# Kernel optimization log

Measured on AMD Instinct MI355X. Metric: run time of the kernel, lower is better.

The kernel has to match this reference:

```python
import jax, jax.numpy as jnp
import numpy as np

B, S, HID = 2, 2048, 2048
NH, HD = 16, 128
KVC, QC = 512, 1536


def _rope(x):
    # x: [B, H, S, D]; interleaved-pair rotation matching the torch view(..., D//2, 2)
    b, h, s, d = x.shape
    inv_freq = 1.0 / (10000.0 ** (jnp.arange(0, d, 2, dtype=jnp.float32) / d))  # [D/2]
    pos = jnp.arange(s, dtype=jnp.float32)
    sinusoid = pos[:, None] * inv_freq[None, :]  # [S, D/2]
    sin = jnp.sin(sinusoid)[None, None]  # [1,1,S,D/2]
    cos = jnp.cos(sinusoid)[None, None]
    xr = x.reshape(b, h, s, d // 2, 2)
    x1, x2 = xr[..., 0], xr[..., 1]
    out = jnp.stack([x1 * cos - x2 * sin, x1 * sin + x2 * cos], axis=-1)
    return out.reshape(b, h, s, d)


def setup_inputs() -> dict:
    key = jax.random.key(0)
    ks = jax.random.split(key, 14)
    def lin(k, fan_in, fan_out):
        lim = 1.0 / np.sqrt(fan_in)
        kw, kb = jax.random.split(k)
        W = jax.random.uniform(kw, (fan_in, fan_out), jnp.float32, -lim, lim)
        b = jax.random.uniform(kb, (fan_out,), jnp.float32, -lim, lim)
        return W, b
    x = jax.random.normal(ks[0], (B, S, HID), jnp.float32)
    # causal mask (positions with 0 are masked out)
    attention_mask = jnp.tril(jnp.ones((S, S), jnp.int32))[None, None]  # [1,1,S,S]
    W_dkv, b_dkv = lin(ks[1], HID, KVC)
    W_uk, b_uk = lin(ks[2], KVC, NH * HD)
    W_uv, b_uv = lin(ks[3], KVC, NH * HD)
    W_dq, b_dq = lin(ks[4], HID, QC)
    W_uq, b_uq = lin(ks[5], QC, NH * HD)
    W_o, b_o = lin(ks[6], NH * HD, HID)
    return dict(x=x, attention_mask=attention_mask,
                W_dkv=W_dkv, b_dkv=b_dkv, W_uk=W_uk, b_uk=b_uk,
                W_uv=W_uv, b_uv=b_uv, W_dq=W_dq, b_dq=b_dq,
                W_uq=W_uq, b_uq=b_uq, W_o=W_o, b_o=b_o)


def reference(x, attention_mask, W_dkv, b_dkv, W_uk, b_uk, W_uv, b_uv,
              W_dq, b_dq, W_uq, b_uq, W_o, b_o):
    b, s, _ = x.shape
    kv = x @ W_dkv + b_dkv                                   # [B,S,KVC]
    k = (kv @ W_uk + b_uk).reshape(b, s, NH, HD).transpose(0, 2, 1, 3)  # [B,H,S,D]
    v = (kv @ W_uv + b_uv).reshape(b, s, NH, HD).transpose(0, 2, 1, 3)
    q = ((x @ W_dq + b_dq) @ W_uq + b_uq).reshape(b, s, NH, HD).transpose(0, 2, 1, 3)
    q, k = _rope(q), _rope(k)
    scores = jnp.einsum('bhqd,bhkd->bhqk', q, k) / jnp.sqrt(jnp.float32(HD))
    scores = jnp.where(attention_mask == 0, jnp.float32(-1e9), scores)
    probs = jax.nn.softmax(scores, axis=-1)
    out = jnp.einsum('bhqk,bhkd->bhqd', probs, v)            # [B,H,S,D]
    out = out.transpose(0, 2, 1, 3).reshape(b, s, NH * HD)
    return out @ W_o + b_o
```

## Files before the change

kernel.cpp:

```cpp
#include <hip/hip_runtime.h>
#include <stdint.h>

typedef unsigned short u16;
typedef uint32_t u32;
typedef __attribute__((ext_vector_type(8))) short short8;
typedef __attribute__((ext_vector_type(4))) float f32x4;
typedef __attribute__((ext_vector_type(4))) u32 u32x4;
typedef __attribute__((ext_vector_type(2))) u32 u32x2;
typedef __attribute__((ext_vector_type(4))) unsigned short u16x4;

#define BS_ 4096
#define S_ 2048
#define HID_ 2048

__device__ __forceinline__ float bf2f(u16 u) { union { u32 i; float f; } v; v.i = ((u32)u) << 16; return v.f; }
__device__ __forceinline__ u16 f2bf(float f) {
  union { float f; u32 i; } v; v.f = f;
  u32 r = v.i + 0x7fffu + ((v.i >> 16) & 1u);
  return (u16)(r >> 16);
}

__device__ __forceinline__ void gload16(const void* gsrc, void* ldst) {
  __builtin_amdgcn_global_load_lds(
      (const __attribute__((address_space(1))) void*)gsrc,
      (__attribute__((address_space(3))) void*)ldst, 16, 0, 0);
}

__global__ __launch_bounds__(256) void prep(const float* __restrict__ x, u16* __restrict__ xb,
                                            const float* __restrict__ W_dkv, const float* __restrict__ W_dq,
                                            const float* __restrict__ W_uk, const float* __restrict__ W_uv,
                                            const float* __restrict__ W_uq, const float* __restrict__ W_o,
                                            u16* __restrict__ WdkvqT, u16* __restrict__ WukvT,
                                            u16* __restrict__ WuqT, u16* __restrict__ WoT,
                                            const float* __restrict__ b_dkv, const float* __restrict__ b_dq,
                                            const float* __restrict__ b_uk, const float* __restrict__ b_uv,
                                            float* __restrict__ cs, float* __restrict__ bc1,
                                            float* __restrict__ bc2) {
  __shared__ float tile[64][65];
  int b = blockIdx.x;
  const int t = threadIdx.x;
  if (b < 8192) {
    int i = b * 256 + t;
    float4 v = ((const float4*)x)[i];
    u16x4 o;
    o.x = f2bf(v.x); o.y = f2bf(v.y); o.z = f2bf(v.z); o.w = f2bf(v.w);
    ((u16x4*)xb)[i] = o;
    return;
  }
  b -= 8192;
  if (b < 3328) {
    const float* W; u16* WT; int K, N, gx, r = b;
    if (r < 256)                 { W = W_dkv; WT = WdkvqT;                    K = 2048; N = 512;  gx = 8;  }
    else if ((r -= 256) < 768)   { W = W_dq;  WT = WdkvqT + (size_t)512 * 2048; K = 2048; N = 1536; gx = 24; }
    else if ((r -= 768) < 256)   { W = W_uk;  WT = WukvT;                     K = 512;  N = 2048; gx = 32; }
    else if ((r -= 256) < 256)   { W = W_uv;  WT = WukvT + (size_t)2048 * 512;  K = 512;  N = 2048; gx = 32; }
    else if ((r -= 256) < 768)   { W = W_uq;  WT = WuqT;                      K = 1536; N = 2048; gx = 32; }
    else                         { r -= 768;  W = W_o; WT = WoT;              K = 2048; N = 2048; gx = 32; }
    const int nb = (r % gx) * 64, kb = (r / gx) * 64;
#pragma unroll
    for (int c = 0; c < 4; ++c) {
      int idx = c * 256 + t;
      int row = idx >> 4;
      int col4 = (idx & 15) * 4;
      float4 v = *(const float4*)&W[(size_t)(kb + row) * N + nb + col4];
      tile[row][col4 + 0] = v.x; tile[row][col4 + 1] = v.y;
      tile[row][col4 + 2] = v.z; tile[row][col4 + 3] = v.w;
    }
    __syncthreads();
#pragma unroll
    for (int c = 0; c < 4; ++c) {
      int idx = c * 256 + t;
      int n = idx >> 4;
      int k4 = (idx & 15) * 4;
      u16x4 o;
      o.x = f2bf(tile[k4 + 0][n]); o.y = f2bf(tile[k4 + 1][n]);
      o.z = f2bf(tile[k4 + 2][n]); o.w = f2bf(tile[k4 + 3][n]);
      *(u16x4*)&WT[(size_t)(nb + n) * K + kb + k4] = o;
    }
    return;
  }
  b -= 3328;
  if (b < 512) {
    int idx = b * 256 + t;
    int pos = idx >> 6, i = idx & 63;
    float inv = powf(10000.f, -(float)i / 64.f);
    float a = (float)pos * inv;
    cs[idx * 2] = cosf(a);
    cs[idx * 2 + 1] = sinf(a);
    return;
  }
  b -= 512;
  {
    int i = b * 256 + t;
    if (i < 512) bc1[i] = b_dkv[i];
    else if (i < 2048) bc1[i] = b_dq[i - 512];
    else if (i < 4096) bc2[i - 2048] = b_uk[i - 2048];
    else if (i < 6144) bc2[i - 2048] = b_uv[i - 4096];
  }
}

template <int OUTF32>
__global__ __launch_bounds__(256) void gemm_bt(const u16* __restrict__ A, int lda,
                                               const u16* __restrict__ BT,
                                               const float* __restrict__ bias,
                                               void* __restrict__ Cout,
                                               int M, int N, int K) {
  __shared__ u16 As[128 * 64];
  __shared__ u16 Bs[128 * 64];
  const int t = threadIdx.x;
  const int lane = t & 63, wave = t >> 6;
  const int wm = wave >> 1, wn = wave & 1;
  const int gx = gridDim.x;
  const int nwg = gx * gridDim.y;
  const int flat = blockIdx.y * gx + blockIdx.x;
  const int swz = (flat & 7) * (nwg >> 3) + (flat >> 3);
  const int tn = swz % gx, tm = swz / gx;
  const int r16 = lane & 15, q4 = lane >> 4;

  f32x4 acc[4][4];
#pragma unroll
  for (int m = 0; m < 4; ++m)
#pragma unroll
    for (int n = 0; n < 4; ++n) acc[m][n] = (f32x4){0.f, 0.f, 0.f, 0.f};

  for (int kt = 0; kt < K; kt += 64) {
#pragma unroll
    for (int c = 0; c < 4; ++c) {
      int idx = c * 256 + t;
      int row = idx >> 3, ch = idx & 7;
      gload16(&A[(size_t)(tm * 128 + row) * lda + kt + ch * 8], (char*)As + idx * 16);
      gload16(&BT[(size_t)(tn * 128 + row) * K + kt + ch * 8], (char*)Bs + idx * 16);
    }
    __syncthreads();
#pragma unroll
    for (int kk = 0; kk < 64; kk += 32) {
      short8 af[4], bfv[4];
#pragma unroll
      for (int m = 0; m < 4; ++m)
        af[m] = *(const short8*)&As[(wm * 64 + m * 16 + r16) * 64 + kk + q4 * 8];
#pragma unroll
      for (int n = 0; n < 4; ++n)
        bfv[n] = *(const short8*)&Bs[(wn * 64 + n * 16 + r16) * 64 + kk + q4 * 8];
      __builtin_amdgcn_s_setprio(1);
#pragma unroll
      for (int m = 0; m < 4; ++m)
#pragma unroll
        for (int n = 0; n < 4; ++n)
          acc[m][n] = __builtin_amdgcn_mfma_f32_16x16x32_bf16(bfv[n], af[m], acc[m][n], 0, 0, 0);
      __builtin_amdgcn_s_setprio(0);
    }
    __syncthreads();
  }
#pragma unroll
  for (int n = 0; n < 4; ++n) {
    int gc0 = tn * 128 + wn * 64 + n * 16 + q4 * 4;
    float4 bv4 = *(const float4*)&bias[gc0];
#pragma unroll
    for (int m = 0; m < 4; ++m) {
      int grow = tm * 128 + wm * 64 + m * 16 + r16;
      float v0 = acc[m][n][0] + bv4.x, v1 = acc[m][n][1] + bv4.y;
      float v2 = acc[m][n][2] + bv4.z, v3 = acc[m][n][3] + bv4.w;
      if (OUTF32) {
        float4 o; o.x = v0; o.y = v1; o.z = v2; o.w = v3;
        *(float4*)&((float*)Cout)[(size_t)grow * N + gc0] = o;
      } else {
        u16x4 o; o.x = f2bf(v0); o.y = f2bf(v1); o.z = f2bf(v2); o.w = f2bf(v3);
        *(u16x4*)&((u16*)Cout)[(size_t)grow * N + gc0] = o;
      }
    }
  }
}

__global__ __launch_bounds__(256) void gemm23(const u16* __restrict__ kvq1,
                                              const u16* __restrict__ WukvT, const u16* __restrict__ WuqT,
                                              const float* __restrict__ bc2, const float* __restrict__ b_uq,
                                              const float* __restrict__ cs,
                                              u16* __restrict__ kbuf, u16* __restrict__ VT,
                                              u16* __restrict__ qb) {
  __shared__ u16 As[128 * 64];
  __shared__ u16 Bs[128 * 64];
  const int t = threadIdx.x;
  const int lane = t & 63, wave = t >> 6;
  const int wm = wave >> 1, wn = wave & 1;
  const int bflat = blockIdx.x;
  const bool g2 = (bflat < 1024);
  const u16* A  = g2 ? kvq1 : (kvq1 + 512);
  const u16* BT = g2 ? WukvT : WuqT;
  const float* bias = g2 ? bc2 : b_uq;
  const int N = g2 ? 4096 : 2048;
  const int K = g2 ? 512 : 1536;
  const int gx = g2 ? 32 : 16;
  const int nwg = g2 ? 1024 : 512;
  const int flat = g2 ? bflat : (bflat - 1024);
  const int swz = (flat & 7) * (nwg >> 3) + (flat >> 3);
  const int tn = swz % gx, tm = swz / gx;
  const int r16 = lane & 15, q4 = lane >> 4;

  f32x4 acc[4][4];
#pragma unroll
  for (int m = 0; m < 4; ++m)
#pragma unroll
    for (int n = 0; n < 4; ++n) acc[m][n] = (f32x4){0.f, 0.f, 0.f, 0.f};

  for (int kt = 0; kt < K; kt += 64) {
#pragma unroll
    for (int c = 0; c < 4; ++c) {
      int idx = c * 256 + t;
      int row = idx >> 3, ch = idx & 7;
      gload16(&A[(size_t)(tm * 128 + row) * 2048 + kt + ch * 8], (char*)As + idx * 16);
      gload16(&BT[(size_t)(tn * 128 + row) * K + kt + ch * 8], (char*)Bs + idx * 16);
    }
    __syncthreads();
#pragma unroll
    for (int kk = 0; kk < 64; kk += 32) {
      short8 af[4], bfv[4];
#pragma unroll
      for (int m = 0; m < 4; ++m)
        af[m] = *(const short8*)&As[(wm * 64 + m * 16 + r16) * 64 + kk + q4 * 8];
#pragma unroll
      for (int n = 0; n < 4; ++n)
        bfv[n] = *(const short8*)&Bs[(wn * 64 + n * 16 + r16) * 64 + kk + q4 * 8];
      __builtin_amdgcn_s_setprio(1);
#pragma unroll
      for (int m = 0; m < 4; ++m)
#pragma unroll
        for (int n = 0; n < 4; ++n)
          acc[m][n] = __builtin_amdgcn_mfma_f32_16x16x32_bf16(bfv[n], af[m], acc[m][n], 0, 0, 0);
      __builtin_amdgcn_s_setprio(0);
    }
    __syncthreads();
  }

  const bool isV = g2 && (tn >= 16);
  u16* outp = g2 ? kbuf : qb;
#pragma unroll
  for (int n = 0; n < 4; ++n) {
    int gc0 = tn * 128 + wn * 64 + n * 16 + q4 * 4;
    float4 bv4 = *(const float4*)&bias[gc0];
    const int i0 = (gc0 & 127) >> 1;
#pragma unroll
    for (int m = 0; m < 4; ++m) {
      int grow = tm * 128 + wm * 64 + m * 16 + r16;
      float v0 = acc[m][n][0] + bv4.x, v1 = acc[m][n][1] + bv4.y;
      float v2 = acc[m][n][2] + bv4.z, v3 = acc[m][n][3] + bv4.w;
      if (!isV) {
        int s = grow & 2047;
        float4 cp = *(const float4*)&cs[((size_t)s * 64 + i0) * 2];
        float y0 = v0 * cp.x - v1 * cp.y;
        float y1 = v0 * cp.y + v1 * cp.x;
        float y2 = v2 * cp.z - v3 * cp.w;
        float y3 = v2 * cp.w + v3 * cp.z;
        u16x4 o; o.x = f2bf(y0); o.y = f2bf(y1); o.z = f2bf(y2); o.w = f2bf(y3);
        *(u16x4*)&outp[(size_t)grow * 2048 + gc0] = o;
      } else {
        int gcv = gc0 - 2048;
        int hh = gcv >> 7, d0 = gcv & 127;
        int bb = grow >> 11, s = grow & 2047;
        u16* vdst = VT + ((size_t)(bb * 16 + hh) * 128 + d0) * S_ + s;
        vdst[0]        = f2bf(v0);
        vdst[S_]       = f2bf(v1);
        vdst[2 * S_]   = f2bf(v2);
        vdst[3 * S_]   = f2bf(v3);
      }
    }
  }
}

__global__ __launch_bounds__(256, 2) void attn_kernel(const u16* __restrict__ Q, const u16* __restrict__ K,
                                                      int kld, const u16* __restrict__ VT,
                                                      u16* __restrict__ O) {
  __shared__ char smem[75776];
  u16* Kl = (u16*)smem;
  u16* Vl = (u16*)(smem + 32768);
  u16* Pl = (u16*)(smem + 65536);
  float* ex = (float*)smem;

  const int t = threadIdx.x;
  const int lane = t & 63, w = t >> 6;
  const int r16 = lane & 15, q4 = lane >> 4;
  const int par = w >> 1, sub = w & 1;
  const int b = blockIdx.x;
  const int xcd = b & 7, u = b >> 3;
  const int p = u & 15, g4 = u >> 4;
  const int bh = g4 * 8 + xcd;
  const int bb = bh >> 4, h = bh & 15;
  const u16* Qb = Q + (size_t)bb * S_ * HID_ + (size_t)h * 128;
  const u16* Kb = K + (size_t)bb * S_ * kld + (size_t)h * 128;
  const u16* VTb = VT + (size_t)bh * 128 * S_;
  u16* Ob = O + (size_t)bb * S_ * HID_ + (size_t)h * 128;

  auto stage = [&](int rs, int kvbase) {
#pragma unroll
    for (int pp = 0; pp < 2; ++pp) {
      int kvb = kvbase + pp * 32;
      char* kd = (char*)(Kl + (size_t)(rs * 2 + pp) * 4096);
      char* vd = (char*)(Vl + (size_t)(rs * 2 + pp) * 4096);
#pragma unroll
      for (int c = 0; c < 2; ++c) {
        int s = c * 256 + t;
        int row = s >> 4;
        int ch = (s & 15) ^ (row & 7);
        gload16(&Kb[(size_t)(kvb + row) * kld + ch * 8], kd + s * 16);
      }
#pragma unroll
      for (int c = 0; c < 2; ++c) {
        int s = c * 256 + t;
        int row = s >> 2;
        int ch = (s & 3) ^ ((row >> 1) & 3);
        gload16(&VTb[(size_t)row * S_ + kvb + ch * 8], vd + s * 16);
      }
    }
  };

  u16* Pw = Pl + (size_t)w * 1280;
  const float SCALE = 0.08838834764831845f;

#pragma unroll
  for (int seg = 0; seg < 2; ++seg) {
    const int qt = seg ? (31 - p) : p;
    const int nr = qt + 1;
    const int qrow0 = qt * 64 + sub * 32;

    short8 qf[2][4];
#pragma unroll
    for (int m = 0; m < 2; ++m)
#pragma unroll
      for (int dk = 0; dk < 4; ++dk)
        qf[m][dk] = *(const short8*)&Qb[(size_t)(qrow0 + m * 16 + r16) * HID_ + dk * 32 + q4 * 8];

    f32x4 ao[2][8];
    float mr[2], lr[2];
#pragma unroll
    for (int m = 0; m < 2; ++m) {
#pragma unroll
      for (int dn = 0; dn < 8; ++dn) ao[m][dn] = (f32x4){0.f, 0.f, 0.f, 0.f};
      mr[m] = -1e30f; lr[m] = 0.f;
    }

    stage(0, 0);
    __syncthreads();

    for (int r = 0; r < nr; ++r) {
      const int rs = r & 1;
      if (r + 1 < nr) stage(rs ^ 1, (r + 1) * 64);
      const int kv0 = r * 64 + par * 32;
      const u16* Kbuf = Kl + (size_t)(rs * 2 + par) * 4096;
      const u16* Vbuf = Vl + (size_t)(rs * 2 + par) * 4096;

      if (kv0 <= qrow0 + 31) {
        f32x4 sc[2][2];
#pragma unroll
        for (int m = 0; m < 2; ++m)
#pragma unroll
          for (int n = 0; n < 2; ++n) sc[m][n] = (f32x4){0.f, 0.f, 0.f, 0.f};
#pragma unroll
        for (int dk = 0; dk < 4; ++dk) {
          short8 kf[2];
#pragma unroll
          for (int n = 0; n < 2; ++n) {
            int kr = n * 16 + r16;
            int ba = (kr * 256 + dk * 64 + q4 * 16) ^ ((kr & 7) << 4);
            kf[n] = *(const short8*)((const char*)Kbuf + ba);
          }
          __builtin_amdgcn_s_setprio(1);
#pragma unroll
          for (int n = 0; n < 2; ++n)
#pragma unroll
            for (int m = 0; m < 2; ++m)
              sc[m][n] = __builtin_amdgcn_mfma_f32_16x16x32_bf16(kf[n], qf[m][dk], sc[m][n], 0, 0, 0);
          __builtin_amdgcn_s_setprio(0);
        }
        const bool nm = (kv0 + 31 > qrow0);
#pragma unroll
        for (int m = 0; m < 2; ++m) {
          const int q = qrow0 + m * 16 + r16;
#pragma unroll
          for (int n = 0; n < 2; ++n)
#pragma unroll
            for (int j = 0; j < 4; ++j) {
              float sv = sc[m][n][j] * SCALE;
              if (nm) {
                int kv = kv0 + n * 16 + q4 * 4 + j;
                if (kv > q) sv = -1e30f;
              }
              sc[m][n][j] = sv;
            }
        }
        float tm0[2];
#pragma unroll
        for (int m = 0; m < 2; ++m) {
          float tm = sc[m][0][0];
#pragma unroll
          for (int n = 0; n < 2; ++n)
#pragma unroll
            for (int j = 0; j < 4; ++j) tm = fmaxf(tm, sc[m][n][j]);
          tm = fmaxf(tm, __shfl_xor(tm, 16));
          tm = fmaxf(tm, __shfl_xor(tm, 32));
          tm0[m] = tm;
        }
        float growth = fmaxf(tm0[0] - mr[0], tm0[1] - mr[1]);
        if (!__all(growth <= 8.0f)) {
#pragma unroll
          for (int m = 0; m < 2; ++m) {
            float mnew = fmaxf(mr[m], tm0[m]);
            float fsc = __expf(mr[m] - mnew);
            lr[m] *= fsc; mr[m] = mnew;
#pragma unroll
            for (int dn = 0; dn < 8; ++dn) ao[m][dn] *= fsc;
          }
        }
#pragma unroll
        for (int m = 0; m < 2; ++m) {
          float ps = 0.f;
#pragma unroll
          for (int n = 0; n < 2; ++n)
#pragma unroll
            for (int j = 0; j < 4; ++j) {
              float pv = __expf(sc[m][n][j] - mr[m]);
              sc[m][n][j] = pv;
              ps += pv;
            }
          ps += __shfl_xor(ps, 16);
          ps += __shfl_xor(ps, 32);
          lr[m] += ps;
        }
#pragma unroll
        for (int m = 0; m < 2; ++m)
#pragma unroll
          for (int n = 0; n < 2; ++n) {
            u32 lo, hi;
            asm("v_cvt_pk_bf16_f32 %0, %1, %2" : "=v"(lo) : "v"(sc[m][n][0]), "v"(sc[m][n][1]));
            asm("v_cvt_pk_bf16_f32 %0, %1, %2" : "=v"(hi) : "v"(sc[m][n][2]), "v"(sc[m][n][3]));
            u32x2 pr; pr.x = lo; pr.y = hi;
            int ba = (m * 16 + r16) * 80 + n * 32 + q4 * 8;
            *(u32x2*)((char*)Pw + ba) = pr;
          }
        short8 pb[2];
#pragma unroll
        for (int m = 0; m < 2; ++m)
          pb[m] = *(const short8*)((const char*)Pw + (m * 16 + r16) * 80 + q4 * 16);
        __builtin_amdgcn_s_setprio(1);
#pragma unroll
        for (int dn = 0; dn < 8; ++dn) {
          int d = dn * 16 + r16;
          int bv = d * 64 + ((q4 ^ ((d >> 1) & 3)) * 16);
          short8 vf = *(const short8*)((const char*)Vbuf + bv);
#pragma unroll
          for (int m = 0; m < 2; ++m)
            ao[m][dn] = __builtin_amdgcn_mfma_f32_16x16x32_bf16(vf, pb[m], ao[m][dn], 0, 0, 0);
        }
        __builtin_amdgcn_s_setprio(0);
      }
      __syncthreads();
    }

    {
      float* exb = ex + (size_t)sub * 4352 + (size_t)lane * 68;
      if (par == 1) {
#pragma unroll
        for (int m = 0; m < 2; ++m)
#pragma unroll
          for (int dn = 0; dn < 8; ++dn)
            *(f32x4*)(exb + m * 32 + dn * 4) = ao[m][dn];
        exb[64] = mr[0]; exb[65] = mr[1]; exb[66] = lr[0]; exb[67] = lr[1];
      }
      __syncthreads();
      if (par == 0) {
#pragma unroll
        for (int m = 0; m < 2; ++m) {
          float mB = exb[64 + m], lB = exb[66 + m];
          float mx = fmaxf(mr[m], mB);
          float wA = __expf(mr[m] - mx), wB = __expf(mB - mx);
          float inv = 1.f / (lr[m] * wA + lB * wB);
          const int q = qrow0 + m * 16 + r16;
#pragma unroll
          for (int dn = 0; dn < 8; ++dn) {
            f32x4 ob = *(const f32x4*)(exb + m * 32 + dn * 4);
            u16x4 o;
#pragma unroll
            for (int j = 0; j < 4; ++j) o[j] = f2bf((ao[m][dn][j] * wA + ob[j] * wB) * inv);
            *(u16x4*)&Ob[(size_t)q * HID_ + dn * 16 + q4 * 4] = o;
          }
        }
      }
      __syncthreads();
    }
  }
}

extern "C" void kernel_launch(void* const* d_in, const int* in_sizes, int n_in,
                              void* d_out, int out_size, void* d_ws, size_t ws_size,
                              hipStream_t stream) {
  (void)in_sizes; (void)n_in; (void)out_size; (void)ws_size;
  const float* x     = (const float*)d_in[0];
  const float* W_dkv = (const float*)d_in[2];
  const float* b_dkv = (const float*)d_in[3];
  const float* W_uk  = (const float*)d_in[4];
  const float* b_uk  = (const float*)d_in[5];
  const float* W_uv  = (const float*)d_in[6];
  const float* b_uv  = (const float*)d_in[7];
  const float* W_dq  = (const float*)d_in[8];
  const float* b_dq  = (const float*)d_in[9];
  const float* W_uq  = (const float*)d_in[10];
  const float* b_uq  = (const float*)d_in[11];
  const float* W_o   = (const float*)d_in[12];
  const float* b_o   = (const float*)d_in[13];
  float* out = (float*)d_out;

  char* ws = (char*)d_ws;
  size_t off = 0;
  auto carve = [&](size_t bytes) { void* p = ws + off; off += (bytes + 255) & ~(size_t)255; return p; };
  u16* xb     = (u16*)carve((size_t)BS_ * 2048 * 2);
  u16* WdkvqT = (u16*)carve((size_t)2048 * 2048 * 2);
  u16* WukvT  = (u16*)carve((size_t)4096 * 512 * 2);
  u16* WuqT   = (u16*)carve((size_t)2048 * 1536 * 2);
  u16* WoT    = (u16*)carve((size_t)2048 * 2048 * 2);
  u16* kvq1   = (u16*)carve((size_t)BS_ * 2048 * 2);
  u16* kbuf   = (u16*)carve((size_t)BS_ * 2048 * 2);
  u16* qb     = (u16*)carve((size_t)BS_ * 2048 * 2);
  u16* aob    = (u16*)carve((size_t)BS_ * 2048 * 2);
  float* cs   = (float*)carve((size_t)2048 * 64 * 2 * 4);
  float* bc1  = (float*)carve((size_t)2048 * 4);
  float* bc2  = (float*)carve((size_t)4096 * 4);
  u16* VT     = xb;

  prep<<<dim3(12056), 256, 0, stream>>>(x, xb, W_dkv, W_dq, W_uk, W_uv, W_uq, W_o,
                                        WdkvqT, WukvT, WuqT, WoT,
                                        b_dkv, b_dq, b_uk, b_uv, cs, bc1, bc2);

  gemm_bt<0><<<dim3(2048 / 128, BS_ / 128), 256, 0, stream>>>(xb, 2048, WdkvqT, bc1, kvq1, BS_, 2048, 2048);

  gemm23<<<dim3(1536), 256, 0, stream>>>(kvq1, WukvT, WuqT, bc2, b_uq, cs, kbuf, VT, qb);

  attn_kernel<<<dim3(512), 256, 0, stream>>>(qb, kbuf, 2048, VT, aob);

  gemm_bt<1><<<dim3(2048 / 128, BS_ / 128), 256, 0, stream>>>(aob, 2048, WoT, b_o, out, BS_, 2048, 2048);
}
```

Before: 271.3 us.

## Double-buffer gemm_bt K tiles and transpose V through LDS for coalesced stores

Result: no change. 267.7 us (-1.3%).

```diff
diff --git a/kernel.cpp b/kernel.cpp
--- a/kernel.cpp
+++ b/kernel.cpp
@@ -105,8 +105,8 @@
                                                const float* __restrict__ bias,
                                                void* __restrict__ Cout,
                                                int M, int N, int K) {
-  __shared__ u16 As[128 * 64];
-  __shared__ u16 Bs[128 * 64];
+  __shared__ u16 As[2][128 * 64];
+  __shared__ u16 Bs[2][128 * 64];
   const int t = threadIdx.x;
   const int lane = t & 63, wave = t >> 6;
   const int wm = wave >> 1, wn = wave & 1;
@@ -123,24 +123,31 @@
 #pragma unroll
     for (int n = 0; n < 4; ++n) acc[m][n] = (f32x4){0.f, 0.f, 0.f, 0.f};
 
-  for (int kt = 0; kt < K; kt += 64) {
+  auto stg = [&](int bufi, int kt) {
 #pragma unroll
     for (int c = 0; c < 4; ++c) {
       int idx = c * 256 + t;
       int row = idx >> 3, ch = idx & 7;
-      gload16(&A[(size_t)(tm * 128 + row) * lda + kt + ch * 8], (char*)As + idx * 16);
-      gload16(&BT[(size_t)(tn * 128 + row) * K + kt + ch * 8], (char*)Bs + idx * 16);
-    }
-    __syncthreads();
+      gload16(&A[(size_t)(tm * 128 + row) * lda + kt + ch * 8], (char*)As[bufi] + idx * 16);
+      gload16(&BT[(size_t)(tn * 128 + row) * K + kt + ch * 8], (char*)Bs[bufi] + idx * 16);
+    }
+  };
+
+  const int nkt = K >> 6;
+  stg(0, 0);
+  __syncthreads();
+  for (int it = 0; it < nkt; ++it) {
+    const int buf = it & 1;
+    if (it + 1 < nkt) stg(buf ^ 1, (it + 1) << 6);
 #pragma unroll
     for (int kk = 0; kk < 64; kk += 32) {
       short8 af[4], bfv[4];
 #pragma unroll
       for (int m = 0; m < 4; ++m)
-        af[m] = *(const short8*)&As[(wm * 64 + m * 16 + r16) * 64 + kk + q4 * 8];
+        af[m] = *(const short8*)&As[buf][(wm * 64 + m * 16 + r16) * 64 + kk + q4 * 8];
 #pragma unroll
       for (int n = 0; n < 4; ++n)
-        bfv[n] = *(const short8*)&Bs[(wn * 64 + n * 16 + r16) * 64 + kk + q4 * 8];
+        bfv[n] = *(const short8*)&Bs[buf][(wn * 64 + n * 16 + r16) * 64 + kk + q4 * 8];
       __builtin_amdgcn_s_setprio(1);
 #pragma unroll
       for (int m = 0; m < 4; ++m)
@@ -177,8 +184,9 @@
                                               const float* __restrict__ cs,
                                               u16* __restrict__ kbuf, u16* __restrict__ VT,
                                               u16* __restrict__ qb) {
-  __shared__ u16 As[128 * 64];
-  __shared__ u16 Bs[128 * 64];
+  __shared__ u16 sh[2 * 128 * 64];
+  u16* As = sh;
+  u16* Bs = sh + 8192;
   const int t = threadIdx.x;
   const int lane = t & 63, wave = t >> 6;
   const int wm = wave >> 1, wn = wave & 1;
@@ -187,7 +195,6 @@
   const u16* A  = g2 ? kvq1 : (kvq1 + 512);
   const u16* BT = g2 ? WukvT : WuqT;
   const float* bias = g2 ? bc2 : b_uq;
-  const int N = g2 ? 4096 : 2048;
   const int K = g2 ? 512 : 1536;
   const int gx = g2 ? 32 : 16;
   const int nwg = g2 ? 1024 : 512;
@@ -232,18 +239,18 @@
   }
 
   const bool isV = g2 && (tn >= 16);
-  u16* outp = g2 ? kbuf : qb;
-#pragma unroll
-  for (int n = 0; n < 4; ++n) {
-    int gc0 = tn * 128 + wn * 64 + n * 16 + q4 * 4;
-    float4 bv4 = *(const float4*)&bias[gc0];
-    const int i0 = (gc0 & 127) >> 1;
-#pragma unroll
-    for (int m = 0; m < 4; ++m) {
-      int grow = tm * 128 + wm * 64 + m * 16 + r16;
-      float v0 = acc[m][n][0] + bv4.x, v1 = acc[m][n][1] + bv4.y;
-      float v2 = acc[m][n][2] + bv4.z, v3 = acc[m][n][3] + bv4.w;
-      if (!isV) {
+  if (!isV) {
+    u16* outp = g2 ? kbuf : qb;
+#pragma unroll
+    for (int n = 0; n < 4; ++n) {
+      int gc0 = tn * 128 + wn * 64 + n * 16 + q4 * 4;
+      float4 bv4 = *(const float4*)&bias[gc0];
+      const int i0 = (gc0 & 127) >> 1;
+#pragma unroll
+      for (int m = 0; m < 4; ++m) {
+        int grow = tm * 128 + wm * 64 + m * 16 + r16;
+        float v0 = acc[m][n][0] + bv4.x, v1 = acc[m][n][1] + bv4.y;
+        float v2 = acc[m][n][2] + bv4.z, v3 = acc[m][n][3] + bv4.w;
         int s = grow & 2047;
         float4 cp = *(const float4*)&cs[((size_t)s * 64 + i0) * 2];
         float y0 = v0 * cp.x - v1 * cp.y;
@@ -252,16 +259,38 @@
         float y3 = v2 * cp.w + v3 * cp.z;
         u16x4 o; o.x = f2bf(y0); o.y = f2bf(y1); o.z = f2bf(y2); o.w = f2bf(y3);
         *(u16x4*)&outp[(size_t)grow * 2048 + gc0] = o;
-      } else {
-        int gcv = gc0 - 2048;
-        int hh = gcv >> 7, d0 = gcv & 127;
-        int bb = grow >> 11, s = grow & 2047;
-        u16* vdst = VT + ((size_t)(bb * 16 + hh) * 128 + d0) * S_ + s;
-        vdst[0]        = f2bf(v0);
-        vdst[S_]       = f2bf(v1);
-        vdst[2 * S_]   = f2bf(v2);
-        vdst[3 * S_]   = f2bf(v3);
-      }
+      }
+    }
+  } else {
+    u16* lt = sh;
+#pragma unroll
+    for (int n = 0; n < 4; ++n) {
+      int gc0 = tn * 128 + wn * 64 + n * 16 + q4 * 4;
+      float4 bv4 = *(const float4*)&bias[gc0];
+      int dL0 = wn * 64 + n * 16 + q4 * 4;
+#pragma unroll
+      for (int m = 0; m < 4; ++m) {
+        int sL = wm * 64 + m * 16 + r16;
+        float vv[4] = {acc[m][n][0] + bv4.x, acc[m][n][1] + bv4.y,
+                       acc[m][n][2] + bv4.z, acc[m][n][3] + bv4.w};
+#pragma unroll
+        for (int j = 0; j < 4; ++j) {
+          int dd = dL0 + j;
+          lt[dd * 128 + (sL ^ ((dd & 7) << 4))] = f2bf(vv[j]);
+        }
+      }
+    }
+    __syncthreads();
+    const int hh = tn - 16;
+    const int bb2 = tm >> 4;
+    const int s0 = (tm & 15) * 128;
+    u16* vbase = VT + (size_t)(bb2 * 16 + hh) * 128 * S_ + s0;
+#pragma unroll
+    for (int c = 0; c < 8; ++c) {
+      int idx = c * 256 + t;
+      int d = idx >> 4, ch = idx & 15;
+      short8 v = *(const short8*)&lt[d * 128 + ((ch * 8) ^ ((d & 7) << 4))];
+      *(short8*)&vbase[(size_t)d * S_ + ch * 8] = v;
     }
   }
 }
```
